# Performance work log

Hardware: AMD Instinct MI355X
Metric: run time of the kernel (lower is better)

Reference implementation:

```python
import math
import jax, jax.numpy as jnp
import numpy as np

EMBED = 256
HEADS = 8
LEVELS = 4
POINTS = 4
HEAD_DIM = EMBED // HEADS
SPATIAL = np.array([[100, 100], [50, 50], [25, 25], [13, 13]], dtype=np.int64)
LV = int((SPATIAL[:, 0] * SPATIAL[:, 1]).sum())  # 13294
BS = 2
LQ = LV


def _offset_bias():
    # matches torch _reset_parameters: directional grid bias for sampling_offsets
    thetas = np.arange(HEADS, dtype=np.float32) * (2.0 * math.pi / HEADS)
    grid = np.stack([np.cos(thetas), np.sin(thetas)], -1)
    grid = grid / np.abs(grid).max(-1, keepdims=True)
    grid = np.tile(grid.reshape(HEADS, 1, 1, 2), (1, LEVELS, POINTS, 1)).astype(np.float32)
    for i in range(POINTS):
        grid[:, :, i, :] *= i + 1
    return jnp.asarray(grid.reshape(-1))


def setup_inputs() -> dict:
    key = jax.random.key(0)
    ks = jax.random.split(key, 7)
    TP = HEADS * LEVELS * POINTS

    def xavier(k, fi, fo):
        lim = math.sqrt(6.0 / (fi + fo))
        return jax.random.uniform(k, (fi, fo), minval=-lim, maxval=lim, dtype=jnp.float32)

    return {
        "query": jax.random.normal(ks[0], (BS, LQ, EMBED), jnp.float32),
        "reference_points": jax.random.uniform(ks[1], (BS, LQ, LEVELS, 2), dtype=jnp.float32),
        "value": jax.random.normal(ks[2], (BS, LV, EMBED), jnp.float32),
        "value_mask": jnp.zeros((BS, LV), dtype=bool),
        "spatial_shapes": SPATIAL,
        "W_off": 0.01 * jax.random.normal(ks[3], (EMBED, TP * 2), jnp.float32),
        "b_off": _offset_bias(),
        "W_attn": 0.01 * jax.random.normal(ks[4], (EMBED, TP), jnp.float32),
        "b_attn": jnp.zeros((TP,), jnp.float32),
        "W_val": xavier(ks[5], EMBED, EMBED),
        "b_val": jnp.zeros((EMBED,), jnp.float32),
        "W_out": xavier(ks[6], EMBED, EMBED),
        "b_out": jnp.zeros((EMBED,), jnp.float32),
    }


def _ms_deform_attn(value, spatial_shapes, sampling_locations, attention_weights):
    # value: [bs, Lv, nH, d]; sampling_locations: [bs, Lq, nH, nL, nP, 2] in [0,1]
    # attention_weights: [bs, Lq, nH, nL, nP]
    bs, Lv, nH, d = value.shape
    Lq, nL, nP = sampling_locations.shape[1], sampling_locations.shape[3], sampling_locations.shape[4]
    out = jnp.zeros((bs, nH, Lq, d), value.dtype)
    start = 0
    for l in range(nL):
        H, W = int(spatial_shapes[l, 0]), int(spatial_shapes[l, 1])
        # level feature map, flat: [bs, nH, H*W, d]
        v = jnp.transpose(value[:, start:start + H * W], (0, 2, 1, 3))
        loc = sampling_locations[:, :, :, l]  # [bs, Lq, nH, nP, 2]
        # grid_sample(align_corners=False): pixel coord = loc * size - 0.5
        x = loc[..., 0] * W - 0.5
        y = loc[..., 1] * H - 0.5
        x0 = jnp.floor(x)
        y0 = jnp.floor(y)
        lw = x - x0  # frac weights
        lh = y - y0
        x0i = x0.astype(jnp.int32)
        y0i = y0.astype(jnp.int32)
        aw = jnp.transpose(attention_weights[:, :, :, l], (0, 2, 1, 3))  # [bs, nH, Lq, nP]
        acc = jnp.zeros((bs, nH, Lq, d), value.dtype)
        for dy, dx, w in ((0, 0, (1 - lh) * (1 - lw)), (0, 1, (1 - lh) * lw),
                          (1, 0, lh * (1 - lw)), (1, 1, lh * lw)):
            xi = x0i + dx
            yi = y0i + dy
            valid = (xi >= 0) & (xi < W) & (yi >= 0) & (yi < H)  # padding_mode='zeros'
            idx = jnp.clip(yi, 0, H - 1) * W + jnp.clip(xi, 0, W - 1)  # [bs, Lq, nH, nP]
            idx_t = jnp.transpose(idx, (0, 2, 1, 3)).reshape(bs, nH, Lq * nP)
            g = jnp.take_along_axis(v, idx_t[..., None], axis=2).reshape(bs, nH, Lq, nP, d)
            wv = (jnp.transpose(w, (0, 2, 1, 3)) * jnp.transpose(valid, (0, 2, 1, 3))) * aw
            acc = acc + jnp.einsum('bhqpd,bhqp->bhqd', g, wv)
        out = out + acc
        start += H * W
    return jnp.transpose(out, (0, 2, 1, 3)).reshape(bs, Lq, nH * d)


def _forward(query, reference_points, value, value_mask, spatial_shapes,
             W_off, b_off, W_attn, b_attn, W_val, b_val, W_out, b_out):
    bs, Lq = query.shape[:2]
    Lv = value.shape[1]
    v = value @ W_val + b_val
    v = jnp.where(value_mask[..., None], 0.0, v)  # masked_fill(mask, 0)
    v = v.reshape(bs, Lv, HEADS, HEAD_DIM)
    off = (query @ W_off + b_off).reshape(bs, Lq, HEADS, LEVELS, POINTS, 2)
    aw = jax.nn.softmax((query @ W_attn + b_attn).reshape(bs, Lq, HEADS, LEVELS * POINTS), axis=-1)
    aw = aw.reshape(bs, Lq, HEADS, LEVELS, POINTS)
    # offset normalizer: (W, H) per level
    norm = jnp.stack([jnp.asarray(spatial_shapes)[:, 1], jnp.asarray(spatial_shapes)[:, 0]], -1).astype(query.dtype)
    loc = reference_points[:, :, None, :, None, :] + off / norm[None, None, None, :, None, :]
    out = _ms_deform_attn(v, spatial_shapes, loc, aw)
    return out @ W_out + b_out


def reference(query, reference_points, value, value_mask, spatial_shapes,
              W_off, b_off, W_attn, b_attn, W_val, b_val, W_out, b_out):
    return _forward(query, reference_points, value, value_mask, spatial_shapes,
                    W_off, b_off, W_attn, b_attn, W_val, b_val, W_out, b_out)
```

## Files before the change

kernel.cpp:

```cpp
#include <hip/hip_runtime.h>
#include <hip/hip_bf16.h>
#include <hip/hip_fp16.h>
#include <stdint.h>

#define EMBED 256
#define HEADS 8
#define LEVELS 4
#define POINTS 4
#define HEAD_DIM 32
#define BS 2
#define LV_TOTAL 13294
#define LQ LV_TOTAL
#define TP 128
#define M_ROWS (BS * LV_TOTAL)
#define QPB 32

typedef __attribute__((ext_vector_type(8))) short bf16x8;
typedef __attribute__((ext_vector_type(4))) float f32x4;

static __device__ __forceinline__ unsigned short f2bf(float x) {
  __hip_bfloat16 h = __float2bfloat16(x);
  return *reinterpret_cast<unsigned short*>(&h);
}
static __device__ __forceinline__ float bf2f(unsigned short u) {
  return __uint_as_float(((unsigned int)u) << 16);
}
static __device__ __forceinline__ unsigned short f2hbits(float x) {
  __half h = __float2half(x);
  return *reinterpret_cast<unsigned short*>(&h);
}

#define MIX(acc, pk, w, vs)                                              \
  asm("v_fma_mix_f32 %0, %1, %2, %0 op_sel:[" #vs                        \
      ",0,0] op_sel_hi:[1,1,0]"                                          \
      : "+v"(acc)                                                        \
      : "v"(pk), "v"(w))

__global__ __launch_bounds__(256) void prep_wt_kernel(
    const float* __restrict__ W_val, const float* __restrict__ W_off,
    const float* __restrict__ W_attn, const float* __restrict__ W_out,
    unsigned short* __restrict__ WT_val, unsigned short* __restrict__ WT_oa,
    unsigned short* __restrict__ WT_out) {
  const int bid = blockIdx.x;
  const int k = threadIdx.x;
  const float* src;
  unsigned short* dst;
  int n, N_src;
  if (bid < 256) {
    src = W_val; dst = WT_val; n = bid; N_src = 256;
  } else if (bid < 512) {
    src = W_off; dst = WT_oa; n = bid - 256; N_src = 256;
  } else if (bid < 640) {
    src = W_attn; dst = WT_oa + 256 * 256; n = bid - 512; N_src = 128;
  } else {
    src = W_out; dst = WT_out; n = bid - 640; N_src = 256;
  }
  dst[n * 256 + k] = f2bf(src[(size_t)k * N_src + n]);
}

template <int NTOT, bool A_BF16, int OUT_MODE, bool MASKED, bool SPLIT_BIAS>
static __device__ __forceinline__ void gemm_body(
    unsigned short* bpanel, const void* __restrict__ Av,
    const unsigned short* __restrict__ BT, const float* __restrict__ bias0,
    const float* __restrict__ bias1, const uint8_t* __restrict__ mask,
    void* __restrict__ Cv, int M, int strip) {
  const int tid = threadIdx.x;
  const int col0 = strip * 64;

#pragma unroll
  for (int it = 0; it < 8; ++it) {
    int c = it * 256 + tid;
    int col = c >> 5;
    int kc = c & 31;
    uint4 vdat = *(const uint4*)(BT + ((size_t)(col0 + col)) * 256 + kc * 8);
    int byteoff = (col << 9) + ((kc << 4) ^ ((col & 7) << 4));
    *(uint4*)((char*)bpanel + byteoff) = vdat;
  }
  __syncthreads();

  const int wave = tid >> 6;
  const int lane = tid & 63;
  const int lr = lane & 15;
  const int kq = lane >> 4;
  const int rowW = blockIdx.x * 128 + wave * 16;
  const int ar0 = min(rowW + lr, M - 1);
  const int ar1 = min(rowW + 64 + lr, M - 1);

  f32x4 acc[2][4];
#pragma unroll
  for (int ri = 0; ri < 2; ++ri)
#pragma unroll
    for (int c = 0; c < 4; ++c) acc[ri][c] = (f32x4){0.f, 0.f, 0.f, 0.f};

  const float* Af = (const float*)Av;
  const unsigned short* Ab = (const unsigned short*)Av;

#pragma unroll
  for (int kk = 0; kk < 8; ++kk) {
    const int k0 = kk * 32 + kq * 8;
    bf16x8 a0, a1;
    if constexpr (A_BF16) {
      a0 = *(const bf16x8*)(Ab + (size_t)ar0 * 256 + k0);
      a1 = *(const bf16x8*)(Ab + (size_t)ar1 * 256 + k0);
    } else {
      float4 p0 = *(const float4*)(Af + (size_t)ar0 * 256 + k0);
      float4 p1 = *(const float4*)(Af + (size_t)ar0 * 256 + k0 + 4);
      float4 p2 = *(const float4*)(Af + (size_t)ar1 * 256 + k0);
      float4 p3 = *(const float4*)(Af + (size_t)ar1 * 256 + k0 + 4);
      a0[0] = (short)f2bf(p0.x); a0[1] = (short)f2bf(p0.y);
      a0[2] = (short)f2bf(p0.z); a0[3] = (short)f2bf(p0.w);
      a0[4] = (short)f2bf(p1.x); a0[5] = (short)f2bf(p1.y);
      a0[6] = (short)f2bf(p1.z); a0[7] = (short)f2bf(p1.w);
      a1[0] = (short)f2bf(p2.x); a1[1] = (short)f2bf(p2.y);
      a1[2] = (short)f2bf(p2.z); a1[3] = (short)f2bf(p2.w);
      a1[4] = (short)f2bf(p3.x); a1[5] = (short)f2bf(p3.y);
      a1[6] = (short)f2bf(p3.z); a1[7] = (short)f2bf(p3.w);
    }
#pragma unroll
    for (int c = 0; c < 4; ++c) {
      const int col = c * 16 + lr;
      const int byteoff = (col << 9) + (((k0 * 2)) ^ ((col & 7) << 4));
      bf16x8 bfrag = *(const bf16x8*)((const char*)bpanel + byteoff);
      acc[0][c] =
          __builtin_amdgcn_mfma_f32_16x16x32_bf16(a0, bfrag, acc[0][c], 0, 0, 0);
      acc[1][c] =
          __builtin_amdgcn_mfma_f32_16x16x32_bf16(a1, bfrag, acc[1][c], 0, 0, 0);
    }
  }

#pragma unroll
  for (int c = 0; c < 4; ++c) {
    const int col = col0 + c * 16 + lr;
    float bv;
    if constexpr (SPLIT_BIAS)
      bv = (col < 256) ? bias0[col] : bias1[col - 256];
    else
      bv = bias0[col];
#pragma unroll
    for (int ri = 0; ri < 2; ++ri) {
#pragma unroll
      for (int i = 0; i < 4; ++i) {
        const int row = rowW + ri * 64 + kq * 4 + i;
        if (row < M) {
          float o = acc[ri][c][i] + bv;
          if constexpr (MASKED) {
            if (mask[row]) o = 0.f;
          }
          if constexpr (OUT_MODE == 0) {
            ((float*)Cv)[(size_t)row * NTOT + col] = o;
          } else if constexpr (OUT_MODE == 1) {
            ((unsigned short*)Cv)[(size_t)row * NTOT + col] = f2bf(o);
          } else if constexpr (OUT_MODE == 2) {
            ((unsigned short*)Cv)[(size_t)(col >> 5) * ((size_t)M * 32) +
                                  (size_t)row * 32 + (col & 31)] = f2hbits(o);
          } else {
            int hh, w_;
            if (col < 256) { hh = col >> 5; w_ = col & 31; }
            else { int c2 = col - 256; hh = c2 >> 4; w_ = 32 + (c2 & 15); }
            ((unsigned short*)Cv)[((size_t)hh * M + row) * 48 + w_] = f2bf(o);
          }
        }
      }
    }
  }
}

__global__ __launch_bounds__(256) void gemm_fused01_kernel(
    const float* __restrict__ value, const float* __restrict__ query,
    const unsigned short* __restrict__ wt_val,
    const unsigned short* __restrict__ wt_oa, const float* __restrict__ b_val,
    const float* __restrict__ b_off, const float* __restrict__ b_attn,
    const uint8_t* __restrict__ mask, unsigned short* __restrict__ vh,
    unsigned short* __restrict__ oah, int M) {
  __shared__ uint4 bpanel4[2048];
  unsigned short* bp = (unsigned short*)bpanel4;
  if (blockIdx.y < 4)
    gemm_body<256, false, 2, true, false>(bp, value, wt_val, b_val, nullptr,
                                          mask, vh, M, blockIdx.y);
  else
    gemm_body<384, false, 3, false, true>(bp, query, wt_oa, b_off, b_attn,
                                          nullptr, oah, M, blockIdx.y - 4);
}

__global__ __launch_bounds__(256) void gemm_out_kernel(
    const unsigned short* __restrict__ o_in,
    const unsigned short* __restrict__ wt_out, const float* __restrict__ b_out,
    float* __restrict__ out, int M) {
  __shared__ uint4 bpanel4[2048];
  unsigned short* bp = (unsigned short*)bpanel4;
  gemm_body<256, true, 0, false, false>(bp, o_in, wt_out, b_out, nullptr,
                                        nullptr, out, M, blockIdx.y);
}

__global__ __launch_bounds__(256) void gather_kernel(
    const float* __restrict__ refpts,
    const __half* __restrict__ vh,
    const unsigned short* __restrict__ oah,
    unsigned short* __restrict__ o_out) {
  __shared__ unsigned short oas[QPB * 48];
  __shared__ float attn_s[QPB][16];
  __shared__ float ref_s[QPB][LEVELS][2];
  __shared__ unsigned int meta_idx[QPB][16];
  __shared__ uint2 meta_w[QPB][16];

  const int qb = blockIdx.x;
  const int h = blockIdx.y;
  const int b = blockIdx.z;
  const int tid = threadIdx.x;

  {
    int row = tid >> 3, j = tid & 7;
    if (j < 6) {
      int qg = min(qb * QPB + row, LQ - 1);
      *(uint4*)(oas + row * 48 + j * 8) = *(const uint4*)(
          oah + ((size_t)h * M_ROWS + (size_t)b * LQ + qg) * 48 + j * 8);
    }
  }
  {
    int q = tid >> 3, rem = tid & 7;
    int qg = min(qb * QPB + q, LQ - 1);
    ref_s[q][rem >> 1][rem & 1] = refpts[((size_t)b * LQ + qg) * 8 + rem];
  }
  __syncthreads();

  if (tid < QPB) {
    const unsigned short* arow = oas + tid * 48 + 32;
    float m = bf2f(arow[0]);
#pragma unroll
    for (int i = 1; i < 16; ++i) m = fmaxf(m, bf2f(arow[i]));
    float ssum = 0.f;
#pragma unroll
    for (int i = 0; i < 16; ++i) {
      float e = __expf(bf2f(arow[i]) - m);
      attn_s[tid][i] = e;
      ssum += e;
    }
    float inv = 1.f / ssum;
#pragma unroll
    for (int i = 0; i < 16; ++i) attn_s[tid][i] *= inv;
  }
  __syncthreads();

#pragma unroll
  for (int pass = 0; pass < 2; ++pass) {
    const int s = pass * 256 + tid;
    const int q = s >> 4, smp = s & 15;
    const int l = smp >> 2, p = smp & 3;
    const int W = (l == 0) ? 100 : (l == 1) ? 50 : (l == 2) ? 25 : 13;
    const int base = (l == 0) ? 0 : (l == 1) ? 10000 : (l == 2) ? 12500 : 13125;
    const float fW = (float)W;

    float ox = bf2f(oas[q * 48 + l * 8 + p * 2]);
    float oy = bf2f(oas[q * 48 + l * 8 + p * 2 + 1]);
    float rx = ref_s[q][l][0], ry = ref_s[q][l][1];
    float aw = attn_s[q][smp];
    float x = fmaf(rx, fW, ox) - 0.5f;
    float y = fmaf(ry, fW, oy) - 0.5f;
    float x0f = floorf(x), y0f = floorf(y);
    float lw = x - x0f, lh = y - y0f;
    int x0 = (int)x0f, y0 = (int)y0f;
    int x1 = x0 + 1, y1 = y0 + 1;
    int xbase = min(max(x0, 0), W - 2);
    bool x0v = (x0 >= 0) && (x0 < W);
    bool x1v = (x1 >= 0) && (x1 < W);
    float ws0 = ((x0v && x0 == xbase) ? (1.f - lw) : 0.f) +
                ((x1v && x1 == xbase) ? lw : 0.f);
    float ws1 = ((x0v && x0 == xbase + 1) ? (1.f - lw) : 0.f) +
                ((x1v && x1 == xbase + 1) ? lw : 0.f);
    bool y0v = (y0 >= 0) && (y0 < W);
    bool y1v = (y1 >= 0) && (y1 < W);
    int yc0 = min(max(y0, 0), W - 1), yc1 = min(max(y1, 0), W - 1);
    float wy0 = y0v ? (1.f - lh) * aw : 0.f;
    float wy1 = y1v ? lh * aw : 0.f;
    const int posx = smp ^ (q & 7);
    meta_w[q][posx] = make_uint2(
        (unsigned int)f2hbits(wy0 * ws0) |
            ((unsigned int)f2hbits(wy0 * ws1) << 16),
        (unsigned int)f2hbits(wy1 * ws0) |
            ((unsigned int)f2hbits(wy1 * ws1) << 16));
    meta_idx[q][posx] = (unsigned int)(yc0 * W + xbase + base) |
                        ((unsigned int)(yc1 * W + xbase + base) << 16);
  }
  __syncthreads();

  {
    const int lane = tid & 63;
    const int wave = tid >> 6;
    const int ql = lane >> 3;
    const int q = wave * 8 + ql;
    const int tp = lane & 7;
    const char* vbase = (const char*)vh +
                        ((size_t)h * M_ROWS + (size_t)b * LV_TOTAL) * 64;
    const unsigned int laneoff =
        (unsigned int)(tp >> 2) * 64 + (unsigned int)(tp & 3) * 16;
    const unsigned int sh = (lane & 4) << 2;

#define PLOAD(C0, C1, IW, WW, smp)                                         \
  {                                                                        \
    const int pos_ = (smp) ^ ql;                                           \
    IW = meta_idx[q][pos_];                                                \
    WW = meta_w[q][pos_];                                                  \
    C0 = *(const uint4*)(vbase + (laneoff + ((IW & 0xffffu) << 6)));       \
    C1 = *(const uint4*)(vbase + (laneoff + ((IW >> 16) << 6)));           \
  }
#define PCONS(C0, C1, WW)                                                  \
  {                                                                        \
    unsigned int wr0 = WW.x >> sh, wr1 = WW.y >> sh;                       \
    MIX(acc[0], C0.x, wr0, 0); MIX(acc[1], C0.x, wr0, 1);                  \
    MIX(acc[2], C0.y, wr0, 0); MIX(acc[3], C0.y, wr0, 1);                  \
    MIX(acc[4], C0.z, wr0, 0); MIX(acc[5], C0.z, wr0, 1);                  \
    MIX(acc[6], C0.w, wr0, 0); MIX(acc[7], C0.w, wr0, 1);                  \
    MIX(acc[0], C1.x, wr1, 0); MIX(acc[1], C1.x, wr1, 1);                  \
    MIX(acc[2], C1.y, wr1, 0); MIX(acc[3], C1.y, wr1, 1);                  \
    MIX(acc[4], C1.z, wr1, 0); MIX(acc[5], C1.z, wr1, 1);                  \
    MIX(acc[6], C1.w, wr1, 0); MIX(acc[7], C1.w, wr1, 1);                  \
  }

    float acc[8];
#pragma unroll
    for (int j = 0; j < 8; ++j) acc[j] = 0.f;

    unsigned int iwA0, iwA1, iwB0, iwB1;
    uint2 wwA0, wwA1, wwB0, wwB1;
    uint4 A00, A01, A10, A11, B00, B01, B10, B11;
    PLOAD(A00, A01, iwA0, wwA0, 0);
    PLOAD(A10, A11, iwA1, wwA1, 1);
#pragma unroll
    for (int it = 0; it < 8; ++it) {
      if (it & 1) {
        if (it < 7) {
          PLOAD(A00, A01, iwA0, wwA0, 2 * it + 2);
          PLOAD(A10, A11, iwA1, wwA1, 2 * it + 3);
        }
        __builtin_amdgcn_sched_barrier(0);
        PCONS(B00, B01, wwB0);
        PCONS(B10, B11, wwB1);
      } else {
        if (it < 7) {
          PLOAD(B00, B01, iwB0, wwB0, 2 * it + 2);
          PLOAD(B10, B11, iwB1, wwB1, 2 * it + 3);
        }
        __builtin_amdgcn_sched_barrier(0);
        PCONS(A00, A01, wwA0);
        PCONS(A10, A11, wwA1);
      }
    }
#undef PLOAD
#undef PCONS

#pragma unroll
    for (int j = 0; j < 8; ++j) acc[j] += __shfl_xor(acc[j], 4, 64);

    const int qg = qb * QPB + q;
    if (((lane & 4) == 0) && qg < LQ) {
      uint4 pk;
      pk.x = (unsigned int)f2bf(acc[0]) | ((unsigned int)f2bf(acc[1]) << 16);
      pk.y = (unsigned int)f2bf(acc[2]) | ((unsigned int)f2bf(acc[3]) << 16);
      pk.z = (unsigned int)f2bf(acc[4]) | ((unsigned int)f2bf(acc[5]) << 16);
      pk.w = (unsigned int)f2bf(acc[6]) | ((unsigned int)f2bf(acc[7]) << 16);
      *(uint4*)(o_out + ((size_t)b * LQ + qg) * EMBED + h * HEAD_DIM +
                (tp & 3) * 8) = pk;
    }
  }
}

extern "C" void kernel_launch(void* const* d_in, const int* in_sizes, int n_in,
                              void* d_out, int out_size, void* d_ws,
                              size_t ws_size, hipStream_t stream) {
  const float* query = (const float*)d_in[0];
  const float* refpts = (const float*)d_in[1];
  const float* value = (const float*)d_in[2];
  const uint8_t* mask = (const uint8_t*)d_in[3];
  const float* W_off = (const float*)d_in[5];
  const float* b_off = (const float*)d_in[6];
  const float* W_attn = (const float*)d_in[7];
  const float* b_attn = (const float*)d_in[8];
  const float* W_val = (const float*)d_in[9];
  const float* b_val = (const float*)d_in[10];
  const float* W_out = (const float*)d_in[11];
  const float* b_out = (const float*)d_in[12];
  float* out = (float*)d_out;

  char* ws = (char*)d_ws;
  unsigned short* vh_ws = (unsigned short*)ws;
  unsigned short* oah_ws =
      (unsigned short*)(ws + 13613056);
  unsigned short* o_ws =
      (unsigned short*)(ws + 13613056 + 20419584);
  unsigned short* wt_val =
      (unsigned short*)(ws + 13613056 + 20419584 + 13613056);
  unsigned short* wt_oa = wt_val + 256 * 256;
  unsigned short* wt_out = wt_oa + 384 * 256;

  prep_wt_kernel<<<896, 256, 0, stream>>>(W_val, W_off, W_attn, W_out, wt_val,
                                          wt_oa, wt_out);

  const int RB = (M_ROWS + 127) / 128;
  gemm_fused01_kernel<<<dim3(RB, 10), 256, 0, stream>>>(
      value, query, wt_val, wt_oa, b_val, b_off, b_attn, mask, vh_ws, oah_ws,
      M_ROWS);

  dim3 g2((LQ + QPB - 1) / QPB, HEADS, BS);
  gather_kernel<<<g2, 256, 0, stream>>>(refpts, (const __half*)vh_ws, oah_ws,
                                        o_ws);

  gemm_out_kernel<<<dim3(RB, 4), 256, 0, stream>>>(o_ws, wt_out, b_out, out,
                                                   M_ROWS);
}
```

Measured before the change: 123.6 us.

## Halve GEMM row tile and prefetch A rows into registers before B-panel staging

The GEMM body now computes 64 rows per block instead of 128, with one 16-row MFMA tile per wave, which doubles the grid. All A-operand loads for the whole K dimension are issued into registers first. The B-panel global loads follow, separated by sched barriers, so A and B loads are in flight together before the LDS store and sync. The cost is more blocks each reloading the same B panel, and higher register use for the prefetched A data (16 uint4 in the fp32 path).

```diff
diff --git a/kernel.cpp b/kernel.cpp
--- a/kernel.cpp
+++ b/kernel.cpp
@@ -66,65 +66,84 @@
     void* __restrict__ Cv, int M, int strip) {
   const int tid = threadIdx.x;
   const int col0 = strip * 64;
-
+  const int wave = tid >> 6;
+  const int lane = tid & 63;
+  const int lr = lane & 15;
+  const int kq = lane >> 4;
+  const int rowW = blockIdx.x * 64 + wave * 16;
+  const int arow = min(rowW + lr, M - 1);
+
+  const float* Af = (const float*)Av;
+  const unsigned short* Ab = (const unsigned short*)Av;
+
+  constexpr int NRA = A_BF16 ? 8 : 16;
+  uint4 ra[NRA];
+  if constexpr (A_BF16) {
+#pragma unroll
+    for (int kk = 0; kk < 8; ++kk)
+      ra[kk] = *(const uint4*)(Ab + (size_t)arow * 256 + kk * 32 + kq * 8);
+  } else {
+#pragma unroll
+    for (int kk = 0; kk < 8; ++kk) {
+      ra[kk * 2] =
+          *(const uint4*)(Af + (size_t)arow * 256 + kk * 32 + kq * 8);
+      ra[kk * 2 + 1] =
+          *(const uint4*)(Af + (size_t)arow * 256 + kk * 32 + kq * 8 + 4);
+    }
+  }
+  __builtin_amdgcn_sched_barrier(0);
+
+  uint4 bst[8];
 #pragma unroll
   for (int it = 0; it < 8; ++it) {
     int c = it * 256 + tid;
     int col = c >> 5;
     int kc = c & 31;
-    uint4 vdat = *(const uint4*)(BT + ((size_t)(col0 + col)) * 256 + kc * 8);
+    bst[it] = *(const uint4*)(BT + ((size_t)(col0 + col)) * 256 + kc * 8);
+  }
+  __builtin_amdgcn_sched_barrier(0);
+
+  bf16x8 afr[8];
+  if constexpr (A_BF16) {
+#pragma unroll
+    for (int kk = 0; kk < 8; ++kk)
+      afr[kk] = __builtin_bit_cast(bf16x8, ra[kk]);
+  } else {
+#pragma unroll
+    for (int kk = 0; kk < 8; ++kk) {
+      float4 p0 = __builtin_bit_cast(float4, ra[kk * 2]);
+      float4 p1 = __builtin_bit_cast(float4, ra[kk * 2 + 1]);
+      afr[kk][0] = (short)f2bf(p0.x); afr[kk][1] = (short)f2bf(p0.y);
+      afr[kk][2] = (short)f2bf(p0.z); afr[kk][3] = (short)f2bf(p0.w);
+      afr[kk][4] = (short)f2bf(p1.x); afr[kk][5] = (short)f2bf(p1.y);
+      afr[kk][6] = (short)f2bf(p1.z); afr[kk][7] = (short)f2bf(p1.w);
+    }
+  }
+
+#pragma unroll
+  for (int it = 0; it < 8; ++it) {
+    int c = it * 256 + tid;
+    int col = c >> 5;
+    int kc = c & 31;
     int byteoff = (col << 9) + ((kc << 4) ^ ((col & 7) << 4));
-    *(uint4*)((char*)bpanel + byteoff) = vdat;
+    *(uint4*)((char*)bpanel + byteoff) = bst[it];
   }
   __syncthreads();
 
-  const int wave = tid >> 6;
-  const int lane = tid & 63;
-  const int lr = lane & 15;
-  const int kq = lane >> 4;
-  const int rowW = blockIdx.x * 128 + wave * 16;
-  const int ar0 = min(rowW + lr, M - 1);
-  const int ar1 = min(rowW + 64 + lr, M - 1);
-
-  f32x4 acc[2][4];
-#pragma unroll
-  for (int ri = 0; ri < 2; ++ri)
-#pragma unroll
-    for (int c = 0; c < 4; ++c) acc[ri][c] = (f32x4){0.f, 0.f, 0.f, 0.f};
-
-  const float* Af = (const float*)Av;
-  const unsigned short* Ab = (const unsigned short*)Av;
+  f32x4 acc[4];
+#pragma unroll
+  for (int c = 0; c < 4; ++c) acc[c] = (f32x4){0.f, 0.f, 0.f, 0.f};
 
 #pragma unroll
   for (int kk = 0; kk < 8; ++kk) {
     const int k0 = kk * 32 + kq * 8;
-    bf16x8 a0, a1;
-    if constexpr (A_BF16) {
-      a0 = *(const bf16x8*)(Ab + (size_t)ar0 * 256 + k0);
-      a1 = *(const bf16x8*)(Ab + (size_t)ar1 * 256 + k0);
-    } else {
-      float4 p0 = *(const float4*)(Af + (size_t)ar0 * 256 + k0);
-      float4 p1 = *(const float4*)(Af + (size_t)ar0 * 256 + k0 + 4);
-      float4 p2 = *(const float4*)(Af + (size_t)ar1 * 256 + k0);
-      float4 p3 = *(const float4*)(Af + (size_t)ar1 * 256 + k0 + 4);
-      a0[0] = (short)f2bf(p0.x); a0[1] = (short)f2bf(p0.y);
-      a0[2] = (short)f2bf(p0.z); a0[3] = (short)f2bf(p0.w);
-      a0[4] = (short)f2bf(p1.x); a0[5] = (short)f2bf(p1.y);
-      a0[6] = (short)f2bf(p1.z); a0[7] = (short)f2bf(p1.w);
-      a1[0] = (short)f2bf(p2.x); a1[1] = (short)f2bf(p2.y);
-      a1[2] = (short)f2bf(p2.z); a1[3] = (short)f2bf(p2.w);
-      a1[4] = (short)f2bf(p3.x); a1[5] = (short)f2bf(p3.y);
-      a1[6] = (short)f2bf(p3.z); a1[7] = (short)f2bf(p3.w);
-    }
 #pragma unroll
     for (int c = 0; c < 4; ++c) {
       const int col = c * 16 + lr;
       const int byteoff = (col << 9) + (((k0 * 2)) ^ ((col & 7) << 4));
       bf16x8 bfrag = *(const bf16x8*)((const char*)bpanel + byteoff);
-      acc[0][c] =
-          __builtin_amdgcn_mfma_f32_16x16x32_bf16(a0, bfrag, acc[0][c], 0, 0, 0);
-      acc[1][c] =
-          __builtin_amdgcn_mfma_f32_16x16x32_bf16(a1, bfrag, acc[1][c], 0, 0, 0);
+      acc[c] = __builtin_amdgcn_mfma_f32_16x16x32_bf16(afr[kk], bfrag, acc[c],
+                                                       0, 0, 0);
     }
   }
 
@@ -137,28 +156,25 @@
     else
       bv = bias0[col];
 #pragma unroll
-    for (int ri = 0; ri < 2; ++ri) {
-#pragma unroll
-      for (int i = 0; i < 4; ++i) {
-        const int row = rowW + ri * 64 + kq * 4 + i;
-        if (row < M) {
-          float o = acc[ri][c][i] + bv;
-          if constexpr (MASKED) {
-            if (mask[row]) o = 0.f;
-          }
-          if constexpr (OUT_MODE == 0) {
-            ((float*)Cv)[(size_t)row * NTOT + col] = o;
-          } else if constexpr (OUT_MODE == 1) {
-            ((unsigned short*)Cv)[(size_t)row * NTOT + col] = f2bf(o);
-          } else if constexpr (OUT_MODE == 2) {
-            ((unsigned short*)Cv)[(size_t)(col >> 5) * ((size_t)M * 32) +
-                                  (size_t)row * 32 + (col & 31)] = f2hbits(o);
-          } else {
-            int hh, w_;
-            if (col < 256) { hh = col >> 5; w_ = col & 31; }
-            else { int c2 = col - 256; hh = c2 >> 4; w_ = 32 + (c2 & 15); }
-            ((unsigned short*)Cv)[((size_t)hh * M + row) * 48 + w_] = f2bf(o);
-          }
+    for (int i = 0; i < 4; ++i) {
+      const int row = rowW + kq * 4 + i;
+      if (row < M) {
+        float o = acc[c][i] + bv;
+        if constexpr (MASKED) {
+          if (mask[row]) o = 0.f;
+        }
+        if constexpr (OUT_MODE == 0) {
+          ((float*)Cv)[(size_t)row * NTOT + col] = o;
+        } else if constexpr (OUT_MODE == 1) {
+          ((unsigned short*)Cv)[(size_t)row * NTOT + col] = f2bf(o);
+        } else if constexpr (OUT_MODE == 2) {
+          ((unsigned short*)Cv)[(size_t)(col >> 5) * ((size_t)M * 32) +
+                                (size_t)row * 32 + (col & 31)] = f2hbits(o);
+        } else {
+          int hh, w_;
+          if (col < 256) { hh = col >> 5; w_ = col & 31; }
+          else { int c2 = col - 256; hh = c2 >> 4; w_ = 32 + (c2 & 15); }
+          ((unsigned short*)Cv)[((size_t)hh * M + row) * 48 + w_] = f2bf(o);
         }
       }
     }
@@ -395,7 +411,7 @@
   prep_wt_kernel<<<896, 256, 0, stream>>>(W_val, W_off, W_attn, W_out, wt_val,
                                           wt_oa, wt_out);
 
-  const int RB = (M_ROWS + 127) / 128;
+  const int RB = (M_ROWS + 63) / 64;
   gemm_fused01_kernel<<<dim3(RB, 10), 256, 0, stream>>>(
       value, query, wt_val, wt_oa, b_val, b_off, b_attn, mask, vh_ws, oah_ws,
       M_ROWS);
```

Result: slower. 129.7 us (+4.9%).
